# Kernel optimization log

Measured on AMD Instinct MI355X. Metric: run time of the kernel, lower is better.

The kernel has to match this reference:

```python
import jax, jax.numpy as jnp
import numpy as np

N_NODES = 10000
IN_FEATS = 50
HIDDEN = 512
OUT_FEATS = 121
N_EDGES = 160000


def setup_inputs() -> dict:
    key = jax.random.key(0)
    ks = jax.random.split(key, 8)
    x = jax.random.normal(ks[0], (N_NODES, IN_FEATS), dtype=jnp.float32)
    edge_index = jax.random.randint(ks[1], (2, N_EDGES), 0, N_NODES, dtype=jnp.int64)
    # SAGEConv params: lin_l applied to aggregated neighbors (carries bias), lin_r to self.
    def glorot(k, fan_in, fan_out):
        s = jnp.sqrt(6.0 / (fan_in + fan_out))
        return jax.random.uniform(k, (fan_in, fan_out), minval=-s, maxval=s, dtype=jnp.float32)
    W1_l = glorot(ks[2], IN_FEATS, HIDDEN)
    W1_r = glorot(ks[3], IN_FEATS, HIDDEN)
    b1 = jnp.zeros((HIDDEN,), dtype=jnp.float32)
    W2_l = glorot(ks[4], HIDDEN, OUT_FEATS)
    W2_r = glorot(ks[5], HIDDEN, OUT_FEATS)
    b2 = jnp.zeros((OUT_FEATS,), dtype=jnp.float32)
    return {"x": x, "edge_index": edge_index, "W1_l": W1_l, "W1_r": W1_r,
            "b1": b1, "W2_l": W2_l, "W2_r": W2_r, "b2": b2}


def _mean_agg(h, src, dst, n_nodes):
    # gather source features per edge, segment-sum at destination, divide by in-degree
    summed = jax.ops.segment_sum(h[src], dst, num_segments=n_nodes)  # [N, F]
    deg = jax.ops.segment_sum(jnp.ones((src.shape[0],), h.dtype), dst, num_segments=n_nodes)
    return summed / jnp.maximum(deg, 1.0)[:, None]


def _sage_conv(h, src, dst, W_l, W_r, b, n_nodes):
    agg = _mean_agg(h, src, dst, n_nodes)
    return agg @ W_l + h @ W_r + b


def reference(x, edge_index, W1_l, W1_r, b1, W2_l, W2_r, b2):
    src, dst = edge_index[0], edge_index[1]
    n = x.shape[0]
    h = _sage_conv(x, src, dst, W1_l, W1_r, b1, n)
    h = jax.nn.relu(h)
    # dropout is identity in eval mode
    out = _sage_conv(h, src, dst, W2_l, W2_r, b2, n)
    return out
```

## Files before the change

### kernel.cpp

```cpp
#include <hip/hip_runtime.h>
#include <hip/hip_bf16.h>

constexpr int NN   = 10000;
constexpr int INF  = 50;
constexpr int HID  = 512;
constexpr int OUTF = 121;
constexpr int NE   = 160000;
constexpr int DMAX = 64;

typedef __attribute__((ext_vector_type(8))) short short8;
typedef __attribute__((ext_vector_type(4))) float floatx4;

__device__ inline float bf2f(unsigned short u) {
    union { unsigned int i; float f; } v; v.i = ((unsigned)u) << 16; return v.f;
}
__device__ inline unsigned short f2bf(float f) {
    __hip_bfloat16 h = __float2bfloat16(f);
    return *(unsigned short*)&h;
}


__global__ __launch_bounds__(256) void k_prep(const float* __restrict__ x,
                                              const float* __restrict__ W1l, const float* __restrict__ W1r,
                                              const float* __restrict__ W2l, const float* __restrict__ W2r,
                                              int* __restrict__ cursor, __hip_bfloat16* __restrict__ xp,
                                              __hip_bfloat16* __restrict__ B1p, __hip_bfloat16* __restrict__ B2p) {
    int idx = blockIdx.x * 256 + threadIdx.x;
    if (idx < NN) cursor[idx] = 0;
    if (idx < 65536) {
        int j = idx & 7, L = (idx >> 3) & 63, kt = (idx >> 9) & 3, nt = idx >> 11;
        int k = kt * 32 + ((L >> 4) * 8 + j);
        int n = nt * 16 + (L & 15);
        float v = (k < 50) ? W1l[k * HID + n] : ((k < 100) ? W1r[(k - 50) * HID + n] : 0.f);
        B1p[idx] = __float2bfloat16(v);
    }
    {
        int j = idx & 7, L = (idx >> 3) & 63, kt = (idx >> 9) & 15, nt = idx >> 13;
        int k = kt * 32 + ((L >> 4) * 8 + j);
        int n = nt * 16 + (L & 15);
        float v;
        if (n < 128) v = (n < OUTF) ? W2l[k * OUTF + n] : 0.f;
        else { int c = n - 128; v = (c < OUTF) ? W2r[k * OUTF + c] : 0.f; }
        B2p[idx] = __float2bfloat16(v);
    }
    for (int r = idx; r < NN * 64; r += 131072) {
        int n = r >> 6, c = r & 63;
        xp[r] = __float2bfloat16(c < INF ? x[n * INF + c] : 0.f);
    }
}


__global__ __launch_bounds__(256) void k_fill(const int* __restrict__ srcv, const int* __restrict__ dstv,
                                              int* __restrict__ cursor, int* __restrict__ csr) {
    int e = blockIdx.x * 256 + threadIdx.x;
    if (e < NE) {
        int d = dstv[e];
        if ((unsigned)d < (unsigned)NN) {
            int pos = atomicAdd(&cursor[d], 1);
            int s = srcv[e];
            s = min(max(s, 0), NN - 1);
            if (pos < DMAX) csr[d * DMAX + pos] = s;
        }
    }
}


__global__ __launch_bounds__(256) void k_fused(const __hip_bfloat16* __restrict__ xp,
                                               const int* __restrict__ cursor, const int* __restrict__ csr,
                                               const __hip_bfloat16* __restrict__ B1p,
                                               const float* __restrict__ b1,
                                               const __hip_bfloat16* __restrict__ B2p,
                                               __hip_bfloat16* __restrict__ Pb, float* __restrict__ Q) {
    __shared__ __align__(16) unsigned short As[16 * 136];
    __shared__ __align__(16) unsigned short Ht[16 * 520];
    int t = threadIdx.x;
    int w = t >> 6, lane = t & 63, quad = lane >> 4, l16 = lane & 15;
    int m0 = blockIdx.x * 16;
    const unsigned short* xs = (const unsigned short*)xp;

#pragma unroll
    for (int p = 0; p < 4; ++p) {
        int nl = w * 4 + p, n = m0 + nl;
        int dt = cursor[n];
        int d = min(dt, DMAX);
        int ids = csr[n * DMAX + lane];
        float s0 = 0.f, s1 = 0.f, s2 = 0.f, s3 = 0.f;
        int j = 0;
        for (; j + 4 <= d; j += 4) {
            int a = __shfl(ids, j), b = __shfl(ids, j + 1), c = __shfl(ids, j + 2), e = __shfl(ids, j + 3);
            s0 += bf2f(xs[a * 64 + lane]);
            s1 += bf2f(xs[b * 64 + lane]);
            s2 += bf2f(xs[c * 64 + lane]);
            s3 += bf2f(xs[e * 64 + lane]);
        }
        for (; j < d; ++j) {
            int a = __shfl(ids, j);
            s0 += bf2f(xs[a * 64 + lane]);
        }
        float s = (s0 + s1) + (s2 + s3);
        float invd = (dt > 0) ? 1.f / (float)dt : 1.f;
        unsigned short self = xs[n * 64 + lane];
        if (lane < INF) As[nl * 136 + lane] = f2bf(s * invd);
        As[nl * 136 + 50 + lane] = self;
        if (lane < 7) *(unsigned*)&As[nl * 136 + 114 + 2 * lane] = 0u;
    }
    __syncthreads();

    short8 af[4];
#pragma unroll
    for (int ks = 0; ks < 4; ++ks) af[ks] = *(const short8*)&As[l16 * 136 + ks * 32 + quad * 8];
    {
        floatx4 acc[8];
#pragma unroll
        for (int nt = 0; nt < 8; ++nt) acc[nt] = floatx4{0.f, 0.f, 0.f, 0.f};
#pragma unroll
        for (int nt = 0; nt < 8; ++nt) {
            int ntile = w * 8 + nt;
            const short* Bb = (const short*)B1p + (ntile * 4 * 64 + lane) * 8;
#pragma unroll
            for (int ks = 0; ks < 4; ++ks) {
                short8 bf = *(const short8*)(Bb + ks * 512);
                acc[nt] = __builtin_amdgcn_mfma_f32_16x16x32_bf16(af[ks], bf, acc[nt], 0, 0, 0);
            }
        }
#pragma unroll
        for (int nt = 0; nt < 8; ++nt) {
            int col = w * 128 + nt * 16 + l16;
            float bias = b1[col];
#pragma unroll
            for (int r = 0; r < 4; ++r)
                Ht[(quad * 4 + r) * 520 + col] = f2bf(fmaxf(acc[nt][r] + bias, 0.f));
        }
    }
    __syncthreads();

    int isQ = w >> 1;
    int halfcol = (w & 1) * 64;
    int tbase = isQ * 8 + (w & 1) * 4;
    floatx4 acc[4];
#pragma unroll
    for (int nt = 0; nt < 4; ++nt) acc[nt] = floatx4{0.f, 0.f, 0.f, 0.f};
#pragma unroll 4
    for (int ks = 0; ks < 16; ++ks) {
        short8 a2 = *(const short8*)&Ht[l16 * 520 + ks * 32 + quad * 8];
#pragma unroll
        for (int nt = 0; nt < 4; ++nt) {
            const short* Bb = (const short*)B2p + (((tbase + nt) * 16 + ks) * 64 + lane) * 8;
            short8 bf = *(const short8*)Bb;
            acc[nt] = __builtin_amdgcn_mfma_f32_16x16x32_bf16(a2, bf, acc[nt], 0, 0, 0);
        }
    }
    if (!isQ) {
#pragma unroll
        for (int nt = 0; nt < 4; ++nt)
#pragma unroll
            for (int r = 0; r < 4; ++r) {
                int row = m0 + quad * 4 + r;
                Pb[row * 128 + halfcol + nt * 16 + l16] = __float2bfloat16(acc[nt][r]);
            }
    } else {
#pragma unroll
        for (int nt = 0; nt < 4; ++nt)
#pragma unroll
            for (int r = 0; r < 4; ++r) {
                int row = m0 + quad * 4 + r;
                Q[row * 128 + halfcol + nt * 16 + l16] = acc[nt][r];
            }
    }
}


__global__ __launch_bounds__(256) void k_final(const __hip_bfloat16* __restrict__ Pb,
                                               const float* __restrict__ Q, const float* __restrict__ b2,
                                               const int* __restrict__ cursor, const int* __restrict__ csr,
                                               float* __restrict__ out) {
    int lane = threadIdx.x & 63;
    int n = blockIdx.x * 4 + (threadIdx.x >> 6);
    int dt = cursor[n];
    int d = min(dt, DMAX);
    int ids = csr[n * DMAX + lane];
    const unsigned* Pw = (const unsigned*)Pb;
    float lo0 = 0.f, lo1 = 0.f, lo2 = 0.f, lo3 = 0.f;
    float hi0 = 0.f, hi1 = 0.f, hi2 = 0.f, hi3 = 0.f;
    int j = 0;
    for (; j + 4 <= d; j += 4) {
        int a = __shfl(ids, j), b = __shfl(ids, j + 1), c = __shfl(ids, j + 2), e = __shfl(ids, j + 3);
        unsigned w0 = Pw[a * 64 + lane];
        unsigned w1 = Pw[b * 64 + lane];
        unsigned w2 = Pw[c * 64 + lane];
        unsigned w3 = Pw[e * 64 + lane];
        lo0 += __uint_as_float(w0 << 16); hi0 += __uint_as_float(w0 & 0xffff0000u);
        lo1 += __uint_as_float(w1 << 16); hi1 += __uint_as_float(w1 & 0xffff0000u);
        lo2 += __uint_as_float(w2 << 16); hi2 += __uint_as_float(w2 & 0xffff0000u);
        lo3 += __uint_as_float(w3 << 16); hi3 += __uint_as_float(w3 & 0xffff0000u);
    }
    for (; j < d; ++j) {
        int a = __shfl(ids, j);
        unsigned w0 = Pw[a * 64 + lane];
        lo0 += __uint_as_float(w0 << 16); hi0 += __uint_as_float(w0 & 0xffff0000u);
    }
    float slo = (lo0 + lo1) + (lo2 + lo3);
    float shi = (hi0 + hi1) + (hi2 + hi3);
    float invd = (dt > 0) ? 1.f / (float)dt : 1.f;
    int c0 = lane * 2, c1 = lane * 2 + 1;
    if (c0 < OUTF) out[n * OUTF + c0] = slo * invd + Q[n * 128 + c0] + b2[c0];
    if (c1 < OUTF) out[n * OUTF + c1] = shi * invd + Q[n * 128 + c1] + b2[c1];
}

extern "C" void kernel_launch(void* const* d_in, const int* in_sizes, int n_in,
                              void* d_out, int out_size, void* d_ws, size_t ws_size,
                              hipStream_t stream) {
    const float* x   = (const float*)d_in[0];
    const int* edges = (const int*)d_in[1];
    const float* W1l = (const float*)d_in[2];
    const float* W1r = (const float*)d_in[3];
    const float* b1  = (const float*)d_in[4];
    const float* W2l = (const float*)d_in[5];
    const float* W2r = (const float*)d_in[6];
    const float* b2  = (const float*)d_in[7];
    float* out = (float*)d_out;

    char* ws = (char*)d_ws;
    int* cursor         = (int*)(ws + 0);
    int* csr            = (int*)(ws + 40000);
    __hip_bfloat16* xp  = (__hip_bfloat16*)(ws + 2600000);
    __hip_bfloat16* Pb  = (__hip_bfloat16*)(ws + 3880000);
    float* Q            = (float*)(ws + 6440000);
    __hip_bfloat16* B1p = (__hip_bfloat16*)(ws + 11560000);
    __hip_bfloat16* B2p = (__hip_bfloat16*)(ws + 11691072);

    const int* srcv = edges;
    const int* dstv = edges + NE;

    k_prep<<<512, 256, 0, stream>>>(x, W1l, W1r, W2l, W2r, cursor, xp, B1p, B2p);
    k_fill<<<625, 256, 0, stream>>>(srcv, dstv, cursor, csr);
    k_fused<<<625, 256, 0, stream>>>(xp, cursor, csr, B1p, b1, B2p, Pb, Q);
    k_final<<<2500, 256, 0, stream>>>(Pb, Q, b2, cursor, csr, out);
}
```

Measured before the change: 127.4 us.

## Double fused-kernel block to 512 threads and use scalar CSR index loads

k_fused now runs 512 threads (8 waves) per block, so each wave gathers 2 nodes instead of 4 and computes fewer output tiles in both GEMM stages. Splitting the work this way is meant to raise wave-level parallelism and hide gather latency. In both gather kernels the neighbor indices are now read through wave-uniform (readfirstlane) addresses, which should allow scalar loads in place of shuffles, and the gather loops are unrolled to 8. The costs are more scalar memory traffic and a larger block, which could limit occupancy.

```diff
diff --git a/kernel.cpp b/kernel.cpp
--- a/kernel.cpp
+++ b/kernel.cpp
@@ -65,12 +65,12 @@
 }
 
 
-__global__ __launch_bounds__(256) void k_fused(const __hip_bfloat16* __restrict__ xp,
-                                               const int* __restrict__ cursor, const int* __restrict__ csr,
-                                               const __hip_bfloat16* __restrict__ B1p,
-                                               const float* __restrict__ b1,
-                                               const __hip_bfloat16* __restrict__ B2p,
-                                               __hip_bfloat16* __restrict__ Pb, float* __restrict__ Q) {
+__global__ __launch_bounds__(512, 4) void k_fused(const __hip_bfloat16* __restrict__ xp,
+                                                  const int* __restrict__ cursor, const int* __restrict__ csr,
+                                                  const __hip_bfloat16* __restrict__ B1p,
+                                                  const float* __restrict__ b1,
+                                                  const __hip_bfloat16* __restrict__ B2p,
+                                                  __hip_bfloat16* __restrict__ Pb, float* __restrict__ Q) {
     __shared__ __align__(16) unsigned short As[16 * 136];
     __shared__ __align__(16) unsigned short Ht[16 * 520];
     int t = threadIdx.x;
@@ -79,27 +79,33 @@
     const unsigned short* xs = (const unsigned short*)xp;
 
 #pragma unroll
-    for (int p = 0; p < 4; ++p) {
-        int nl = w * 4 + p, n = m0 + nl;
-        int dt = cursor[n];
+    for (int p = 0; p < 2; ++p) {
+        int nl = w * 2 + p;
+        int nu = __builtin_amdgcn_readfirstlane(m0 + nl);
+        int dt = cursor[nu];
         int d = min(dt, DMAX);
-        int ids = csr[n * DMAX + lane];
+        const int* crow = csr + nu * DMAX;
         float s0 = 0.f, s1 = 0.f, s2 = 0.f, s3 = 0.f;
         int j = 0;
-        for (; j + 4 <= d; j += 4) {
-            int a = __shfl(ids, j), b = __shfl(ids, j + 1), c = __shfl(ids, j + 2), e = __shfl(ids, j + 3);
-            s0 += bf2f(xs[a * 64 + lane]);
-            s1 += bf2f(xs[b * 64 + lane]);
-            s2 += bf2f(xs[c * 64 + lane]);
-            s3 += bf2f(xs[e * 64 + lane]);
+        for (; j + 8 <= d; j += 8) {
+            int i0 = crow[j], i1 = crow[j + 1], i2 = crow[j + 2], i3 = crow[j + 3];
+            int i4 = crow[j + 4], i5 = crow[j + 5], i6 = crow[j + 6], i7 = crow[j + 7];
+            s0 += bf2f(xs[i0 * 64 + lane]);
+            s1 += bf2f(xs[i1 * 64 + lane]);
+            s2 += bf2f(xs[i2 * 64 + lane]);
+            s3 += bf2f(xs[i3 * 64 + lane]);
+            s0 += bf2f(xs[i4 * 64 + lane]);
+            s1 += bf2f(xs[i5 * 64 + lane]);
+            s2 += bf2f(xs[i6 * 64 + lane]);
+            s3 += bf2f(xs[i7 * 64 + lane]);
         }
         for (; j < d; ++j) {
-            int a = __shfl(ids, j);
-            s0 += bf2f(xs[a * 64 + lane]);
+            int i0 = crow[j];
+            s0 += bf2f(xs[i0 * 64 + lane]);
         }
         float s = (s0 + s1) + (s2 + s3);
         float invd = (dt > 0) ? 1.f / (float)dt : 1.f;
-        unsigned short self = xs[n * 64 + lane];
+        unsigned short self = xs[nu * 64 + lane];
         if (lane < INF) As[nl * 136 + lane] = f2bf(s * invd);
         As[nl * 136 + 50 + lane] = self;
         if (lane < 7) *(unsigned*)&As[nl * 136 + 114 + 2 * lane] = 0u;
@@ -110,12 +116,12 @@
 #pragma unroll
     for (int ks = 0; ks < 4; ++ks) af[ks] = *(const short8*)&As[l16 * 136 + ks * 32 + quad * 8];
     {
-        floatx4 acc[8];
-#pragma unroll
-        for (int nt = 0; nt < 8; ++nt) acc[nt] = floatx4{0.f, 0.f, 0.f, 0.f};
-#pragma unroll
-        for (int nt = 0; nt < 8; ++nt) {
-            int ntile = w * 8 + nt;
+        floatx4 acc[4];
+#pragma unroll
+        for (int nt = 0; nt < 4; ++nt) acc[nt] = floatx4{0.f, 0.f, 0.f, 0.f};
+#pragma unroll
+        for (int nt = 0; nt < 4; ++nt) {
+            int ntile = w * 4 + nt;
             const short* Bb = (const short*)B1p + (ntile * 4 * 64 + lane) * 8;
 #pragma unroll
             for (int ks = 0; ks < 4; ++ks) {
@@ -124,8 +130,8 @@
             }
         }
 #pragma unroll
-        for (int nt = 0; nt < 8; ++nt) {
-            int col = w * 128 + nt * 16 + l16;
+        for (int nt = 0; nt < 4; ++nt) {
+            int col = w * 64 + nt * 16 + l16;
             float bias = b1[col];
 #pragma unroll
             for (int r = 0; r < 4; ++r)
@@ -134,38 +140,35 @@
     }
     __syncthreads();
 
-    int isQ = w >> 1;
-    int halfcol = (w & 1) * 64;
-    int tbase = isQ * 8 + (w & 1) * 4;
-    floatx4 acc[4];
-#pragma unroll
-    for (int nt = 0; nt < 4; ++nt) acc[nt] = floatx4{0.f, 0.f, 0.f, 0.f};
+    int isQ = w >> 2;
+    int wh = w & 3;
+    int tbase = isQ * 8 + wh * 2;
+    floatx4 acc0 = {0.f, 0.f, 0.f, 0.f};
+    floatx4 acc1 = {0.f, 0.f, 0.f, 0.f};
+    const short* Bc0 = (const short*)B2p + ((tbase * 16) * 64 + lane) * 8;
+    const short* Bc1 = (const short*)B2p + (((tbase + 1) * 16) * 64 + lane) * 8;
 #pragma unroll 4
     for (int ks = 0; ks < 16; ++ks) {
         short8 a2 = *(const short8*)&Ht[l16 * 520 + ks * 32 + quad * 8];
-#pragma unroll
-        for (int nt = 0; nt < 4; ++nt) {
-            const short* Bb = (const short*)B2p + (((tbase + nt) * 16 + ks) * 64 + lane) * 8;
-            short8 bf = *(const short8*)Bb;
-            acc[nt] = __builtin_amdgcn_mfma_f32_16x16x32_bf16(a2, bf, acc[nt], 0, 0, 0);
-        }
+        short8 bf0 = *(const short8*)(Bc0 + ks * 512);
+        short8 bf1 = *(const short8*)(Bc1 + ks * 512);
+        acc0 = __builtin_amdgcn_mfma_f32_16x16x32_bf16(a2, bf0, acc0, 0, 0, 0);
+        acc1 = __builtin_amdgcn_mfma_f32_16x16x32_bf16(a2, bf1, acc1, 0, 0, 0);
     }
     if (!isQ) {
 #pragma unroll
-        for (int nt = 0; nt < 4; ++nt)
-#pragma unroll
-            for (int r = 0; r < 4; ++r) {
-                int row = m0 + quad * 4 + r;
-                Pb[row * 128 + halfcol + nt * 16 + l16] = __float2bfloat16(acc[nt][r]);
-            }
+        for (int r = 0; r < 4; ++r) {
+            int row = m0 + quad * 4 + r;
+            Pb[row * 128 + wh * 32 + l16]      = __float2bfloat16(acc0[r]);
+            Pb[row * 128 + wh * 32 + 16 + l16] = __float2bfloat16(acc1[r]);
+        }
     } else {
 #pragma unroll
-        for (int nt = 0; nt < 4; ++nt)
-#pragma unroll
-            for (int r = 0; r < 4; ++r) {
-                int row = m0 + quad * 4 + r;
-                Q[row * 128 + halfcol + nt * 16 + l16] = acc[nt][r];
-            }
+        for (int r = 0; r < 4; ++r) {
+            int row = m0 + quad * 4 + r;
+            Q[row * 128 + wh * 32 + l16]      = acc0[r];
+            Q[row * 128 + wh * 32 + 16 + l16] = acc1[r];
+        }
     }
 }
 
@@ -175,36 +178,45 @@
                                                const int* __restrict__ cursor, const int* __restrict__ csr,
                                                float* __restrict__ out) {
     int lane = threadIdx.x & 63;
-    int n = blockIdx.x * 4 + (threadIdx.x >> 6);
-    int dt = cursor[n];
+    int nu = __builtin_amdgcn_readfirstlane(blockIdx.x * 4 + (threadIdx.x >> 6));
+    int dt = cursor[nu];
     int d = min(dt, DMAX);
-    int ids = csr[n * DMAX + lane];
+    const int* crow = csr + nu * DMAX;
     const unsigned* Pw = (const unsigned*)Pb;
     float lo0 = 0.f, lo1 = 0.f, lo2 = 0.f, lo3 = 0.f;
     float hi0 = 0.f, hi1 = 0.f, hi2 = 0.f, hi3 = 0.f;
     int j = 0;
-    for (; j + 4 <= d; j += 4) {
-        int a = __shfl(ids, j), b = __shfl(ids, j + 1), c = __shfl(ids, j + 2), e = __shfl(ids, j + 3);
-        unsigned w0 = Pw[a * 64 + lane];
-        unsigned w1 = Pw[b * 64 + lane];
-        unsigned w2 = Pw[c * 64 + lane];
-        unsigned w3 = Pw[e * 64 + lane];
+    for (; j + 8 <= d; j += 8) {
+        int i0 = crow[j], i1 = crow[j + 1], i2 = crow[j + 2], i3 = crow[j + 3];
+        int i4 = crow[j + 4], i5 = crow[j + 5], i6 = crow[j + 6], i7 = crow[j + 7];
+        unsigned w0 = Pw[i0 * 64 + lane];
+        unsigned w1 = Pw[i1 * 64 + lane];
+        unsigned w2 = Pw[i2 * 64 + lane];
+        unsigned w3 = Pw[i3 * 64 + lane];
+        unsigned w4 = Pw[i4 * 64 + lane];
+        unsigned w5 = Pw[i5 * 64 + lane];
+        unsigned w6 = Pw[i6 * 64 + lane];
+        unsigned w7 = Pw[i7 * 64 + lane];
         lo0 += __uint_as_float(w0 << 16); hi0 += __uint_as_float(w0 & 0xffff0000u);
         lo1 += __uint_as_float(w1 << 16); hi1 += __uint_as_float(w1 & 0xffff0000u);
         lo2 += __uint_as_float(w2 << 16); hi2 += __uint_as_float(w2 & 0xffff0000u);
         lo3 += __uint_as_float(w3 << 16); hi3 += __uint_as_float(w3 & 0xffff0000u);
+        lo0 += __uint_as_float(w4 << 16); hi0 += __uint_as_float(w4 & 0xffff0000u);
+        lo1 += __uint_as_float(w5 << 16); hi1 += __uint_as_float(w5 & 0xffff0000u);
+        lo2 += __uint_as_float(w6 << 16); hi2 += __uint_as_float(w6 & 0xffff0000u);
+        lo3 += __uint_as_float(w7 << 16); hi3 += __uint_as_float(w7 & 0xffff0000u);
     }
     for (; j < d; ++j) {
-        int a = __shfl(ids, j);
-        unsigned w0 = Pw[a * 64 + lane];
+        int i0 = crow[j];
+        unsigned w0 = Pw[i0 * 64 + lane];
         lo0 += __uint_as_float(w0 << 16); hi0 += __uint_as_float(w0 & 0xffff0000u);
     }
     float slo = (lo0 + lo1) + (lo2 + lo3);
     float shi = (hi0 + hi1) + (hi2 + hi3);
     float invd = (dt > 0) ? 1.f / (float)dt : 1.f;
     int c0 = lane * 2, c1 = lane * 2 + 1;
-    if (c0 < OUTF) out[n * OUTF + c0] = slo * invd + Q[n * 128 + c0] + b2[c0];
-    if (c1 < OUTF) out[n * OUTF + c1] = shi * invd + Q[n * 128 + c1] + b2[c1];
+    if (c0 < OUTF) out[nu * OUTF + c0] = slo * invd + Q[nu * 128 + c0] + b2[c0];
+    if (c1 < OUTF) out[nu * OUTF + c1] = shi * invd + Q[nu * 128 + c1] + b2[c1];
 }
 
 extern "C" void kernel_launch(void* const* d_in, const int* in_sizes, int n_in,
@@ -234,6 +246,6 @@
 
     k_prep<<<512, 256, 0, stream>>>(x, W1l, W1r, W2l, W2r, cursor, xp, B1p, B2p);
     k_fill<<<625, 256, 0, stream>>>(srcv, dstv, cursor, csr);
-    k_fused<<<625, 256, 0, stream>>>(xp, cursor, csr, B1p, b1, B2p, Pb, Q);
+    k_fused<<<625, 512, 0, stream>>>(xp, cursor, csr, B1p, b1, B2p, Pb, Q);
     k_final<<<2500, 256, 0, stream>>>(Pb, Q, b2, cursor, csr, out);
 }
```

Result: faster. 115.5 us (-9.4%).
